# Optimization experiments

Hardware: AMD Instinct MI355X
Metric: run time of the kernel (lower is better)

## Reference

```python
import jax, jax.numpy as jnp
import numpy as np

TEMP = 0.07
BASE_TEMP = 0.07


def setup_inputs() -> dict:
    key = jax.random.key(0)
    k1, k2 = jax.random.split(key)
    B, L, D = 512, 20, 128  # batch, num_classes, feat_size
    features = jax.random.normal(k1, (B, L, D), dtype=jnp.float32)
    # contrastive features are typically L2-normalized projections
    features = features / jnp.linalg.norm(features, axis=-1, keepdims=True)
    labels = jax.random.randint(k2, (B, L), 0, 2).astype(jnp.int32)  # multi-hot
    return {"features": features, "labels": labels}


def reference(features, labels):
    # features: [B, L, D], labels: [B, L] multi-hot
    B, L, D = features.shape
    dt = features.dtype
    lab = labels.astype(dt).T                      # [L, B]
    feat = jnp.transpose(features, (1, 0, 2))      # [L, B, D]

    logits_mask = 1.0 - jnp.eye(B, dtype=dt)       # [B, B], zero diagonal
    # mask[c, i, j] = labels[i, c] * labels[j, c] * (i != j)
    mask = (lab[:, :, None] * lab[:, None, :]) * logits_mask  # [L, B, B]

    # anchor_dot_contrast[c, l, i, j] = f[l,i] . f[c,j] / T  -> exp, masked on (i,j)
    # Compute via one big N x N gram, N = L*B (same math, single GEMM).
    F = feat.reshape(L * B, D)
    E = jnp.exp((F @ F.T) / jnp.asarray(TEMP, dt)).reshape(L, B, L, B)  # E[l,i,c,j]
    tot = E.sum(axis=(0, 3))                       # [B(i), L(c)] : sum over l, all j
    diag = jnp.diagonal(E, axis1=1, axis2=3)       # [L(l), L(c), B(i)] : j == i terms
    # sum_exp_logits[c, i] = sum_{l, j != i} exp(f[l,i].f[c,j]/T)
    S = tot.T - diag.sum(axis=0)                   # [L(c), B(i)]

    # numerator[c, i, j] = f[c,i] . f[c,j] / T
    numerator = jnp.einsum('cid,cjd->cij', feat, feat) / jnp.asarray(TEMP, dt)  # [L,B,B]
    log_prob = numerator - jnp.log(S)[:, :, None]  # [L, B, B]

    mean_log_prob_pos = (mask * log_prob).sum(axis=(0, 2))  # [B]
    average = mask.sum(axis=(0, 2))                          # [B]
    average = jnp.where(average == 0, jnp.asarray(1.0, dt), average)
    mean_log_prob_pos = mean_log_prob_pos / average

    loss = -(TEMP / BASE_TEMP) * jnp.mean(mean_log_prob_pos)
    return loss
```

## Files before the change

### kernel.cpp

```cpp
#include <hip/hip_runtime.h>


#define NB 512
#define NL 20
#define NROW (NB * NL)
#define FBYTES (NROW * 256)
#define SCALE 4.5398160f
#define TEMP_INV 14.285714285714286f

typedef float f32x4 __attribute__((ext_vector_type(4)));
typedef short short8 __attribute__((ext_vector_type(8)));
typedef unsigned short ushort4v __attribute__((ext_vector_type(4)));

static __device__ __forceinline__ unsigned short f2bf(float x) {
  unsigned int b = __float_as_uint(x);
  b += 0x7FFFu + ((b >> 16) & 1u);
  return (unsigned short)(b >> 16);
}

static __device__ __forceinline__ float fexp2(float x) {
#if __has_builtin(__builtin_amdgcn_exp2f)
  return __builtin_amdgcn_exp2f(x);
#else
  return exp2f(x);
#endif
}

__global__ __launch_bounds__(256) void k_prep(const float* __restrict__ feat,
                                              const int* __restrict__ labels,
                                              unsigned char* __restrict__ fswz,
                                              float* __restrict__ gp) {
  const int b = blockIdx.x;
  if (b < 1280) {
    int t = b * 256 + threadIdx.x;
    int q = t & 31;
    int a = t >> 5;
    int l = a >> 9;
    int i = a & 511;
    const float* src = feat + (size_t)i * (NL * 128) + l * 128 + q * 4;
    float4 v = *(const float4*)src;
    ushort4v u;
    u.x = f2bf(v.x * SCALE); u.y = f2bf(v.y * SCALE);
    u.z = f2bf(v.z * SCALE); u.w = f2bf(v.w * SCALE);
    int dst = a * 256 + ((q * 8) ^ ((a & 7) << 4));
    *(ushort4v*)(fswz + dst) = u;
  } else {
    __shared__ float part[2][128];
    const int idx = b - 1280;
    const int c = idx >> 4, grp = idx & 15;
    const int d = threadIdx.x & 127, half = threadIdx.x >> 7;
    const int i0 = grp * 32 + half * 16;
    float s = 0.f;
#pragma unroll
    for (int k = 0; k < 16; ++k) {
      int i = i0 + k;
      s += (float)labels[i * NL + c] * feat[(size_t)i * (NL * 128) + c * 128 + d];
    }
    part[half][d] = s;
    __syncthreads();
    if (half == 0) gp[(c * 16 + grp) * 128 + d] = part[0][d] + part[1][d];
  }
}

__global__ __launch_bounds__(64) void k_gram(const unsigned char* __restrict__ fswz,
                                             float* __restrict__ Pr) {
  __shared__ unsigned char lds[8192];
  const int x = blockIdx.x;
  const int h = x & 1, sr = x >> 1;
  const int c = blockIdx.y;
  const int lane = threadIdx.x;
  const int fr = lane & 15, kg = lane >> 4;
  const int xr = (fr & 7) << 4;

  short8 af[4][4];
#pragma unroll
  for (int kk = 0; kk < 4; ++kk)
#pragma unroll
    for (int m = 0; m < 4; ++m)
      af[kk][m] = *(const short8*)(fswz + (size_t)(sr * 64 + m * 16 + fr) * 256 +
                                   ((kk * 64 + kg * 16) ^ xr));

  const unsigned char* gB = fswz + ((size_t)c * 512 + h * 256) * 256 + lane * 16;
  auto stage = [&](int buf, int t) {
    const unsigned char* g = gB + t * 4096;
    unsigned char* lb = lds + buf * 4096 + lane * 16;
#pragma unroll
    for (int p = 0; p < 4; ++p)
      __builtin_amdgcn_global_load_lds(
          (const __attribute__((address_space(1))) unsigned int*)(g + p * 1024),
          (__attribute__((address_space(3))) unsigned int*)(lb + p * 1024), 16, 0, 0);
  };

  stage(0, 0);
  float esum[4][4] = {};

  const int d8 = sr & 7;
  const bool diagh = ((d8 >> 2) == h);
  const int td0 = (d8 & 3) * 4;

  for (int t = 0; t < 16; ++t) {
    asm volatile("" ::: "memory");
    if (t < 15) {
      stage((t + 1) & 1, t + 1);
      asm volatile("s_waitcnt vmcnt(4)" ::: "memory");
    } else {
      asm volatile("s_waitcnt vmcnt(0)" ::: "memory");
    }

    const unsigned char* lb = lds + (t & 1) * 4096;
    f32x4 acc[4] = {};
#pragma unroll
    for (int kk = 0; kk < 4; ++kk) {
      short8 bf = *(const short8*)(lb + fr * 256 + ((kk * 64 + kg * 16) ^ xr));
#pragma unroll
      for (int m = 0; m < 4; ++m)
        acc[m] = __builtin_amdgcn_mfma_f32_16x16x32_bf16(af[kk][m], bf, acc[m], 0, 0, 0);
    }

    if (diagh && t >= td0 && t < td0 + 4) {
      const int mt = t - td0;
#pragma unroll
      for (int m = 0; m < 4; ++m)
#pragma unroll
        for (int reg = 0; reg < 4; ++reg) {
          float ex = fexp2(acc[m][reg]);
          if (m == mt && (kg * 4 + reg) == fr) ex = 0.f;
          esum[m][reg] += ex;
        }
    } else {
#pragma unroll
      for (int m = 0; m < 4; ++m)
#pragma unroll
        for (int reg = 0; reg < 4; ++reg)
          esum[m][reg] += fexp2(acc[m][reg]);
    }
  }

#pragma unroll
  for (int m = 0; m < 4; ++m)
#pragma unroll
    for (int reg = 0; reg < 4; ++reg) {
      float e = esum[m][reg];
      e += __shfl_xor(e, 1, 64); e += __shfl_xor(e, 2, 64);
      e += __shfl_xor(e, 4, 64); e += __shfl_xor(e, 8, 64);
      if (fr == 0)
        Pr[(((size_t)c * 2 + h) * 160 + sr) * 64 + m * 16 + kg * 4 + reg] = e;
    }
}

__global__ __launch_bounds__(256) void k_ws(const float* __restrict__ Pr,
                                            const float* __restrict__ feat,
                                            const float* __restrict__ gp,
                                            float* __restrict__ Slog,
                                            float* __restrict__ wnum) {
  const int b = blockIdx.x;
  if (b < 2560) {
    const int lane = threadIdx.x & 63;
    const int p = b * 4 + (threadIdx.x >> 6);
    const int c = p >> 9, i = p & 511;
    float2 f = *(const float2*)(feat + (size_t)i * (NL * 128) + c * 128 + lane * 2);
    float gx = 0.f, gy = 0.f;
#pragma unroll
    for (int q = 0; q < 16; ++q) {
      float2 g2 = *(const float2*)(gp + (c * 16 + q) * 128 + lane * 2);
      gx += g2.x; gy += g2.y;
    }
    float v = f.x * gx + f.y * gy;
#pragma unroll
    for (int sh = 1; sh < 64; sh <<= 1) v += __shfl_xor(v, sh, 64);
    if (lane == 0) wnum[p] = (v - 1.f) * TEMP_INV;
  } else {
    int idx = (b - 2560) * 256 + threadIdx.x;
    int c = idx >> 9, i = idx & 511;
    float s = 0.f;
#pragma unroll
    for (int l2 = 0; l2 < NL; ++l2) {
      const float* p2 = Pr + (((size_t)c * 2) * 160 + l2 * 8 + (i >> 6)) * 64 + (i & 63);
      s += p2[0] + p2[160 * 64];
    }
    Slog[idx] = logf(s);
  }
}

__global__ __launch_bounds__(512) void k_final(const float* __restrict__ Slog,
                                               const float* __restrict__ wnum,
                                               const int* __restrict__ labels,
                                               float* __restrict__ out) {
  __shared__ float cnt[NL];
  __shared__ float red[8];
  const int i = threadIdx.x;
  if (i < NL) cnt[i] = 0.f;
  __syncthreads();
  int lab[NL];
#pragma unroll
  for (int cI = 0; cI < NL; ++cI) lab[cI] = labels[i * NL + cI];
#pragma unroll
  for (int cI = 0; cI < NL; ++cI)
    if (lab[cI]) atomicAdd(&cnt[cI], 1.f);
  __syncthreads();
  float avg = 0.f, acc = 0.f;
#pragma unroll
  for (int cI = 0; cI < NL; ++cI) {
    if (lab[cI]) {
      float wgt = cnt[cI] - 1.f;
      avg += wgt;
      acc += wnum[cI * NB + i] - wgt * Slog[cI * NB + i];
    }
  }
  float v = acc / (avg == 0.f ? 1.f : avg);
#pragma unroll
  for (int s = 1; s < 64; s <<= 1) v += __shfl_xor(v, s, 64);
  if ((i & 63) == 0) red[i >> 6] = v;
  __syncthreads();
  if (i == 0) {
    float tot = 0.f;
#pragma unroll
    for (int k = 0; k < 8; ++k) tot += red[k];
    out[0] = -(tot / (float)NB);
  }
}

extern "C" void kernel_launch(void* const* d_in, const int* in_sizes, int n_in,
                              void* d_out, int out_size, void* d_ws, size_t ws_size,
                              hipStream_t stream) {
  const float* feat = (const float*)d_in[0];
  const int* labels = (const int*)d_in[1];
  float* out = (float*)d_out;
  unsigned char* ws = (unsigned char*)d_ws;
  unsigned char* fswz = ws;
  float* Pr = (float*)(ws + FBYTES);
  float* gp = Pr + 20 * 2 * 160 * 64;
  float* Slog = gp + 320 * 128;
  float* wnum = Slog + NROW;

  k_prep<<<1600, 256, 0, stream>>>(feat, labels, fswz, gp);
  dim3 grid(320, 20);
  k_gram<<<grid, 64, 0, stream>>>(fswz, Pr);
  k_ws<<<2600, 256, 0, stream>>>(Pr, feat, gp, Slog, wnum);
  k_final<<<1, 512, 0, stream>>>(Slog, wnum, labels, out);
}
```

Before: 61.61 us.

## Load gram B tiles directly into registers with 4-deep prefetch instead of LDS

Drops the LDS double-buffer staging (global_load_lds plus waitcnt) in the gram kernel. Each lane now loads its B fragments straight from global memory into registers through a 4-slot rotating prefetch queue. Because LDS is no longer read, the XOR swizzle in the prep kernel is removed and the layout becomes linear. Launch bounds request 2 waves per EU. The aim is to cut LDS traffic and synchronisation and to hide latency with deeper register prefetch, at the cost of more VGPRs and uncoalesced 16-byte global loads that depend on L1/L2 hits.

New measurement: 139.1 us. 126% more time.

```diff
diff --git a/kernel.cpp b/kernel.cpp
--- a/kernel.cpp
+++ b/kernel.cpp
@@ -42,8 +42,7 @@
     ushort4v u;
     u.x = f2bf(v.x * SCALE); u.y = f2bf(v.y * SCALE);
     u.z = f2bf(v.z * SCALE); u.w = f2bf(v.w * SCALE);
-    int dst = a * 256 + ((q * 8) ^ ((a & 7) << 4));
-    *(ushort4v*)(fswz + dst) = u;
+    *(ushort4v*)(fswz + a * 256 + q * 8) = u;
   } else {
     __shared__ float part[2][128];
     const int idx = b - 1280;
@@ -62,15 +61,13 @@
   }
 }
 
-__global__ __launch_bounds__(64) void k_gram(const unsigned char* __restrict__ fswz,
-                                             float* __restrict__ Pr) {
-  __shared__ unsigned char lds[8192];
+__global__ __launch_bounds__(64, 2) void k_gram(const unsigned char* __restrict__ fswz,
+                                                float* __restrict__ Pr) {
   const int x = blockIdx.x;
   const int h = x & 1, sr = x >> 1;
   const int c = blockIdx.y;
   const int lane = threadIdx.x;
   const int fr = lane & 15, kg = lane >> 4;
-  const int xr = (fr & 7) << 4;
 
   short8 af[4][4];
 #pragma unroll
@@ -78,63 +75,66 @@
 #pragma unroll
     for (int m = 0; m < 4; ++m)
       af[kk][m] = *(const short8*)(fswz + (size_t)(sr * 64 + m * 16 + fr) * 256 +
-                                   ((kk * 64 + kg * 16) ^ xr));
-
-  const unsigned char* gB = fswz + ((size_t)c * 512 + h * 256) * 256 + lane * 16;
-  auto stage = [&](int buf, int t) {
-    const unsigned char* g = gB + t * 4096;
-    unsigned char* lb = lds + buf * 4096 + lane * 16;
-#pragma unroll
-    for (int p = 0; p < 4; ++p)
-      __builtin_amdgcn_global_load_lds(
-          (const __attribute__((address_space(1))) unsigned int*)(g + p * 1024),
-          (__attribute__((address_space(3))) unsigned int*)(lb + p * 1024), 16, 0, 0);
-  };
-
-  stage(0, 0);
+                                   kk * 64 + kg * 16);
+
+  const unsigned char* gL = fswz + ((size_t)c * 512 + h * 256 + fr) * 256 + kg * 16;
+
+  short8 bq[4][4];
+
+#define ISSUE(SLOT, T)                                                       \
+  {                                                                          \
+    const unsigned char* g_ = gL + (T) * 4096;                               \
+    _Pragma("unroll") for (int q_ = 0; q_ < 4; ++q_)                         \
+        bq[SLOT][q_] = *(const short8*)(g_ + q_ * 64);                       \
+  }
+
   float esum[4][4] = {};
 
   const int d8 = sr & 7;
   const bool diagh = ((d8 >> 2) == h);
   const int td0 = (d8 & 3) * 4;
 
-  for (int t = 0; t < 16; ++t) {
-    asm volatile("" ::: "memory");
-    if (t < 15) {
-      stage((t + 1) & 1, t + 1);
-      asm volatile("s_waitcnt vmcnt(4)" ::: "memory");
-    } else {
-      asm volatile("s_waitcnt vmcnt(0)" ::: "memory");
-    }
-
-    const unsigned char* lb = lds + (t & 1) * 4096;
-    f32x4 acc[4] = {};
-#pragma unroll
-    for (int kk = 0; kk < 4; ++kk) {
-      short8 bf = *(const short8*)(lb + fr * 256 + ((kk * 64 + kg * 16) ^ xr));
-#pragma unroll
-      for (int m = 0; m < 4; ++m)
-        acc[m] = __builtin_amdgcn_mfma_f32_16x16x32_bf16(af[kk][m], bf, acc[m], 0, 0, 0);
-    }
-
-    if (diagh && t >= td0 && t < td0 + 4) {
-      const int mt = t - td0;
-#pragma unroll
-      for (int m = 0; m < 4; ++m)
-#pragma unroll
-        for (int reg = 0; reg < 4; ++reg) {
-          float ex = fexp2(acc[m][reg]);
-          if (m == mt && (kg * 4 + reg) == fr) ex = 0.f;
-          esum[m][reg] += ex;
-        }
-    } else {
-#pragma unroll
-      for (int m = 0; m < 4; ++m)
-#pragma unroll
-        for (int reg = 0; reg < 4; ++reg)
-          esum[m][reg] += fexp2(acc[m][reg]);
-    }
-  }
+#define CONSUME(SLOT, T)                                                     \
+  {                                                                          \
+    f32x4 acc[4] = {};                                                       \
+    _Pragma("unroll") for (int kk = 0; kk < 4; ++kk)                         \
+    _Pragma("unroll") for (int m = 0; m < 4; ++m)                            \
+        acc[m] = __builtin_amdgcn_mfma_f32_16x16x32_bf16(af[kk][m],          \
+                     bq[SLOT][kk], acc[m], 0, 0, 0);                         \
+    const int t_ = (T);                                                      \
+    if (diagh && t_ >= td0 && t_ < td0 + 4) {                                \
+      const int mt = t_ - td0;                                               \
+      _Pragma("unroll") for (int m = 0; m < 4; ++m)                          \
+      _Pragma("unroll") for (int reg = 0; reg < 4; ++reg) {                  \
+        float ex = fexp2(acc[m][reg]);                                       \
+        if (m == mt && (kg * 4 + reg) == fr) ex = 0.f;                       \
+        esum[m][reg] += ex;                                                  \
+      }                                                                      \
+    } else {                                                                 \
+      _Pragma("unroll") for (int m = 0; m < 4; ++m)                          \
+      _Pragma("unroll") for (int reg = 0; reg < 4; ++reg)                    \
+          esum[m][reg] += fexp2(acc[m][reg]);                                \
+    }                                                                        \
+  }
+
+  ISSUE(0, 0)
+  ISSUE(1, 1)
+  ISSUE(2, 2)
+
+  for (int g = 0; g < 3; ++g) {
+    const int t0 = g * 4;
+    ISSUE(3, t0 + 3) CONSUME(0, t0)
+    ISSUE(0, t0 + 4) CONSUME(1, t0 + 1)
+    ISSUE(1, t0 + 5) CONSUME(2, t0 + 2)
+    ISSUE(2, t0 + 6) CONSUME(3, t0 + 3)
+  }
+  ISSUE(3, 15) CONSUME(0, 12)
+  CONSUME(1, 13)
+  CONSUME(2, 14)
+  CONSUME(3, 15)
+
+#undef ISSUE
+#undef CONSUME
 
 #pragma unroll
   for (int m = 0; m < 4; ++m)
```

## Fuse final reduction into k_ws via last-block counter; triple-buffer gram loads

Applied to the files above, without the earlier changes.

Removes the separate single-block k_final launch. The last k_ws block to finish, found with an atomic counter that k_prep resets, now does the final loss reduction over all 512 samples using 256 threads. The gram kernel also moves from double to triple buffering of its LDS B tiles, prefetching two stages ahead to hide load latency. In exchange this adds a threadfence and an atomic per k_ws block and uses more LDS per gram block.

New measurement: 236.4 us. 284% more time.

```diff
diff --git a/kernel.cpp b/kernel.cpp
--- a/kernel.cpp
+++ b/kernel.cpp
@@ -7,6 +7,7 @@
 #define FBYTES (NROW * 256)
 #define SCALE 4.5398160f
 #define TEMP_INV 14.285714285714286f
+#define WS_BLOCKS 2600
 
 typedef float f32x4 __attribute__((ext_vector_type(4)));
 typedef short short8 __attribute__((ext_vector_type(8)));
@@ -29,8 +30,10 @@
 __global__ __launch_bounds__(256) void k_prep(const float* __restrict__ feat,
                                               const int* __restrict__ labels,
                                               unsigned char* __restrict__ fswz,
-                                              float* __restrict__ gp) {
+                                              float* __restrict__ gp,
+                                              unsigned int* __restrict__ ctr) {
   const int b = blockIdx.x;
+  if (b == 0 && threadIdx.x == 0) *ctr = 0u;
   if (b < 1280) {
     int t = b * 256 + threadIdx.x;
     int q = t & 31;
@@ -64,7 +67,7 @@
 
 __global__ __launch_bounds__(64) void k_gram(const unsigned char* __restrict__ fswz,
                                              float* __restrict__ Pr) {
-  __shared__ unsigned char lds[8192];
+  __shared__ unsigned char lds[12288];
   const int x = blockIdx.x;
   const int h = x & 1, sr = x >> 1;
   const int c = blockIdx.y;
@@ -92,7 +95,9 @@
   };
 
   stage(0, 0);
+  stage(1, 1);
   float esum[4][4] = {};
+  int bi = 0;
 
   const int d8 = sr & 7;
   const bool diagh = ((d8 >> 2) == h);
@@ -100,14 +105,17 @@
 
   for (int t = 0; t < 16; ++t) {
     asm volatile("" ::: "memory");
-    if (t < 15) {
-      stage((t + 1) & 1, t + 1);
+    if (t < 14) {
+      int nb = bi + 2; if (nb >= 3) nb -= 3;
+      stage(nb, t + 2);
+      asm volatile("s_waitcnt vmcnt(8)" ::: "memory");
+    } else if (t < 15) {
       asm volatile("s_waitcnt vmcnt(4)" ::: "memory");
     } else {
       asm volatile("s_waitcnt vmcnt(0)" ::: "memory");
     }
 
-    const unsigned char* lb = lds + (t & 1) * 4096;
+    const unsigned char* lb = lds + bi * 4096;
     f32x4 acc[4] = {};
 #pragma unroll
     for (int kk = 0; kk < 4; ++kk) {
@@ -134,6 +142,7 @@
         for (int reg = 0; reg < 4; ++reg)
           esum[m][reg] += fexp2(acc[m][reg]);
     }
+    if (++bi == 3) bi = 0;
   }
 
 #pragma unroll
@@ -151,8 +160,11 @@
 __global__ __launch_bounds__(256) void k_ws(const float* __restrict__ Pr,
                                             const float* __restrict__ feat,
                                             const float* __restrict__ gp,
+                                            const int* __restrict__ labels,
                                             float* __restrict__ Slog,
-                                            float* __restrict__ wnum) {
+                                            float* __restrict__ wnum,
+                                            unsigned int* __restrict__ ctr,
+                                            float* __restrict__ out) {
   const int b = blockIdx.x;
   if (b < 2560) {
     const int lane = threadIdx.x & 63;
@@ -180,44 +192,54 @@
     }
     Slog[idx] = logf(s);
   }
-}
-
-__global__ __launch_bounds__(512) void k_final(const float* __restrict__ Slog,
-                                               const float* __restrict__ wnum,
-                                               const int* __restrict__ labels,
-                                               float* __restrict__ out) {
+
+  __shared__ unsigned int done_s;
+  __threadfence();
+  __syncthreads();
+  if (threadIdx.x == 0) done_s = atomicAdd(ctr, 1u);
+  __syncthreads();
+  if (done_s != WS_BLOCKS - 1) return;
+  __threadfence();
+
   __shared__ float cnt[NL];
-  __shared__ float red[8];
-  const int i = threadIdx.x;
-  if (i < NL) cnt[i] = 0.f;
-  __syncthreads();
-  int lab[NL];
-#pragma unroll
-  for (int cI = 0; cI < NL; ++cI) lab[cI] = labels[i * NL + cI];
-#pragma unroll
-  for (int cI = 0; cI < NL; ++cI)
-    if (lab[cI]) atomicAdd(&cnt[cI], 1.f);
-  __syncthreads();
-  float avg = 0.f, acc = 0.f;
+  __shared__ float red[4];
+  const int tid = threadIdx.x;
+  if (tid < NL) cnt[tid] = 0.f;
+  __syncthreads();
+  int lab0[NL], lab1[NL];
 #pragma unroll
   for (int cI = 0; cI < NL; ++cI) {
-    if (lab[cI]) {
-      float wgt = cnt[cI] - 1.f;
-      avg += wgt;
-      acc += wnum[cI * NB + i] - wgt * Slog[cI * NB + i];
-    }
-  }
-  float v = acc / (avg == 0.f ? 1.f : avg);
-#pragma unroll
-  for (int s = 1; s < 64; s <<= 1) v += __shfl_xor(v, s, 64);
-  if ((i & 63) == 0) red[i >> 6] = v;
-  __syncthreads();
-  if (i == 0) {
-    float tot = 0.f;
-#pragma unroll
-    for (int k = 0; k < 8; ++k) tot += red[k];
-    out[0] = -(tot / (float)NB);
-  }
+    lab0[cI] = labels[tid * NL + cI];
+    lab1[cI] = labels[(tid + 256) * NL + cI];
+  }
+#pragma unroll
+  for (int cI = 0; cI < NL; ++cI) {
+    if (lab0[cI]) atomicAdd(&cnt[cI], 1.f);
+    if (lab1[cI]) atomicAdd(&cnt[cI], 1.f);
+  }
+  __syncthreads();
+  float vs = 0.f;
+#pragma unroll
+  for (int half = 0; half < 2; ++half) {
+    const int i = tid + half * 256;
+    float avg = 0.f, acc = 0.f;
+#pragma unroll
+    for (int cI = 0; cI < NL; ++cI) {
+      int lv = half ? lab1[cI] : lab0[cI];
+      if (lv) {
+        float wgt = cnt[cI] - 1.f;
+        avg += wgt;
+        acc += wnum[cI * NB + i] - wgt * Slog[cI * NB + i];
+      }
+    }
+    vs += acc / (avg == 0.f ? 1.f : avg);
+  }
+#pragma unroll
+  for (int s = 1; s < 64; s <<= 1) vs += __shfl_xor(vs, s, 64);
+  if ((tid & 63) == 0) red[tid >> 6] = vs;
+  __syncthreads();
+  if (tid == 0)
+    out[0] = -((red[0] + red[1] + red[2] + red[3]) / (float)NB);
 }
 
 extern "C" void kernel_launch(void* const* d_in, const int* in_sizes, int n_in,
@@ -232,10 +254,10 @@
   float* gp = Pr + 20 * 2 * 160 * 64;
   float* Slog = gp + 320 * 128;
   float* wnum = Slog + NROW;
-
-  k_prep<<<1600, 256, 0, stream>>>(feat, labels, fswz, gp);
+  unsigned int* ctr = (unsigned int*)(wnum + NROW);
+
+  k_prep<<<1600, 256, 0, stream>>>(feat, labels, fswz, gp, ctr);
   dim3 grid(320, 20);
   k_gram<<<grid, 64, 0, stream>>>(fswz, Pr);
-  k_ws<<<2600, 256, 0, stream>>>(Pr, feat, gp, Slog, wnum);
-  k_final<<<1, 512, 0, stream>>>(Slog, wnum, labels, out);
-}
+  k_ws<<<WS_BLOCKS, 256, 0, stream>>>(Pr, feat, gp, labels, Slog, wnum, ctr, out);
+}
```
